# Performance work log

Measured on AMD Instinct MI355X. Metric: run time of the kernel, lower is better.

## Reference

```python
import jax, jax.numpy as jnp
import numpy as np
from jax.scipy.special import logsumexp

NG, NF, NR, NW = 5, 5, 5, 4
STEP = 1 + NG + NF + NR            # 16 signatures per writer
M_OTH = NG + NF + NR               # comparisons per writer
MARGIN, RANDOM_MARGIN = 1.0, 1.5
ALPHA, BETA, P_W, R_W = 0.1, 1.0, 0.01, 0.01
GAMMA = 5.0                        # SoftDTW(gamma=5, bandwidth=int(0.1)=0 -> full DTW)
KNUM, KMUL = 5, 2.0
MAXLEN, FEAT = 512, 64
BIG = 1e10                         # finite stand-in for +inf (exp(-BIG/GAMMA) == 0 in f32)


def _pairwise_sqdist(X, Y):
    # X,Y: (B, L, F) -> (B, L, L) squared euclidean cost (SoftDTW distance func)
    xy = jnp.einsum('bif,bjf->bij', X, Y)
    d = (X * X).sum(-1)[:, :, None] + (Y * Y).sum(-1)[:, None, :] - 2.0 * xy
    return jnp.maximum(d, 0.0)


def _soft_dtw(D, la, lb):
    # Batched soft-DTW via anti-diagonal scan. Padded DP is causal, so
    # R[la, lb] only depends on D[:la, :lb]; padding never contaminates it.
    B, L, _ = D.shape
    ii = jnp.arange(1, L + 1)
    r2 = jnp.full((B, L + 1), BIG, D.dtype).at[:, 0].set(0.0)  # diag d=0: R[0,0]=0
    r1 = jnp.full((B, L + 1), BIG, D.dtype)                    # diag d=1: borders

    def step(carry, d):
        rp2, rp1 = carry
        j = d - ii
        valid = (j >= 1) & (j <= L)
        jc = jnp.clip(j, 1, L)
        Dd = D[:, ii - 1, jc - 1]                               # (B, L)
        # softmin(R[i-1,j], R[i,j-1], R[i-1,j-1]) = -g*logsumexp(-r/g)
        stack = jnp.stack([-rp1[:, :-1], -rp1[:, 1:], -rp2[:, :-1]]) / GAMMA
        smin = -GAMMA * logsumexp(stack, axis=0)
        vals = jnp.where(valid[None, :], Dd + smin, BIG)
        r_new = jnp.concatenate([jnp.full((B, 1), BIG, D.dtype), vals], axis=1)
        return (rp1, r_new), r_new

    _, R = jax.lax.scan(step, (r2, r1), jnp.arange(2, 2 * L + 1))
    # R: (2L-1, B, L+1); diag d stored at d-2, R[la, lb] sits at index la
    return R[la + lb - 2, jnp.arange(B), la]


def _mmd(src, tgt):
    # DAN-style multi-kernel gaussian MMD; signatures flattened to vectors
    b = src.shape[0]
    total = jnp.concatenate([src, tgt], axis=0)
    n = total.shape[0]
    sq = (total * total).sum(-1)
    l2 = jnp.maximum(sq[:, None] + sq[None, :] - 2.0 * (total @ total.T), 0.0)
    bw = jax.lax.stop_gradient(l2.sum()) / (n * n - n)
    bw = bw / KMUL ** (KNUM // 2)
    bws = bw * KMUL ** jnp.arange(KNUM, dtype=total.dtype)
    k = jnp.exp(-l2[None] / bws[:, None, None]).sum(0)
    return jnp.mean(k[:b, :b] + k[b:, b:] - k[:b, b:] - k[b:, :b])


def _forward(data, lens):
    w = jnp.arange(NW)
    anchor_idx = jnp.repeat(w * STEP, M_OTH)
    other_idx = (w[:, None] * STEP + 1 + jnp.arange(M_OTH)[None, :]).reshape(-1)
    D = _pairwise_sqdist(data[anchor_idx], data[other_idx])
    la, lb = lens[anchor_idx], lens[other_idx]
    r = _soft_dtw(D, la, lb)
    dists = (r / (la + lb).astype(data.dtype)).reshape(NW, M_OTH)  # avg pooling
    dist_g = dists[:, :NG]
    dist_n = dists[:, NG:]
    lk_s = jax.nn.relu(dist_g[:, :, None] + MARGIN - dist_n[:, None, :NF])
    lk_r = jax.nn.relu(dist_g[:, :, None] + RANDOM_MARGIN - dist_n[:, None, NF:])
    ca = dist_g.mean(1)
    cb = dist_n[:, :NW].mean(1)            # quirk of original: first nw negatives
    intra = (dist_g - ca[:, None]).sum(1)  # identically 0, kept for fidelity
    inter = jax.nn.relu(BETA - jnp.abs(ca - cb))
    nz_s = (lk_s > 0).sum((1, 2))
    nz_r = (lk_r > 0).sum((1, 2))
    lv = (lk_s.sum((1, 2)) + lk_r.sum((1, 2))) / (nz_s + nz_r + 1)
    # BCE over softmin pairs (dist_g[0], dist_r[j]) vs targets (1, 0):
    # softmin gives sm0 = sigmoid(dr - dg0); BCE = -(log sm0 + log(1-sm1))/2 = -log sm0
    logits = dist_n[:, NF:] - dist_g[:, 0:1]
    bce = -jnp.mean(jax.nn.log_sigmoid(logits), axis=1)
    total_loss = jnp.mean(bce + lv + intra * P_W + inter * R_W)
    # pairwise MMD over writers (i in 0..nw-1, j in 1..nw-1, i != j), nr random excluded
    pairs = np.array([(i, j) for i in range(NW) for j in range(1, NW) if i != j])
    seg = data.reshape(NW, STEP, MAXLEN, FEAT)[:, :STEP - NR]
    seg = seg.reshape(NW, STEP - NR, MAXLEN * FEAT)
    mmd_vals = jax.vmap(_mmd)(seg[pairs[:, 0]], seg[pairs[:, 1]])
    siz = NW * (NW + 1) // 2
    mmds = jnp.zeros((siz,), data.dtype).at[:pairs.shape[0]].set(mmd_vals)
    mmd1 = jnp.max(mmds) * ALPHA
    return total_loss + mmd1, nz_r.sum()


def setup_inputs():
    key = jax.random.key(0)
    k1, k2, k3 = jax.random.split(key, 3)
    data = jax.random.normal(k1, (NW * STEP, MAXLEN, FEAT), dtype=jnp.float32)
    lens = jax.random.randint(k2, (NW * STEP,), MAXLEN // 2, MAXLEN + 1, dtype=jnp.int32)
    target = jax.random.randint(k3, (NW * STEP,), 0, NW, dtype=jnp.int32)
    return {"data": data, "lens": lens, "target": target, "n_classes": 100}


def reference(data, lens, target, n_classes):
    # target / n_classes are unused in the original forward (sms is dead code)
    return _forward(data, lens)
```

## Files before the change

kernel.cpp:

```cpp
#include <hip/hip_runtime.h>
#include <math.h>

#define NG 5
#define NF 5
#define NR 5
#define NW 4
#define STEP 16
#define M_OTH 15
#define NB 60
#define L 512
#define FEAT 64
#define GAMMA 5.0f
#define SEGN 11
#define NSEG 44
#define SEGD 32768

#define C1   0.28853900817779268f
#define GLN2 3.4657359027997265f
#define BIGS 2.8853900e9f
#define BNDW 792
#define GRAM_BLK0 60

__global__ __launch_bounds__(256, 2) void sqdist_kernel(const float* __restrict__ data,
                                                        float* __restrict__ DS) {
    int b = blockIdx.z;
    int w = b / M_OTH, m = b % M_OTH;
    const float* X = data + (size_t)(w * STEP) * L * FEAT;
    const float* Y = data + (size_t)(w * STEP + 1 + m) * L * FEAT;
    int ti = blockIdx.y * 128;
    int tj = blockIdx.x * 128;

    __shared__ float Xs[128][68];
    __shared__ float Ys[128][68];
    __shared__ float nx[128], ny[128];

    int t = threadIdx.y * 16 + threadIdx.x;
    #pragma unroll
    for (int k = 0; k < 8; ++k) {
        int idx = t + k * 256;
        int r = idx >> 4, c = (idx & 15) * 4;
        *(float4*)&Xs[r][c] = *(const float4*)(X + (size_t)(ti + r) * FEAT + c);
        *(float4*)&Ys[r][c] = *(const float4*)(Y + (size_t)(tj + r) * FEAT + c);
    }
    __syncthreads();
    {
        int r = t & 127;
        const float* row = (t < 128) ? Xs[r] : Ys[r];
        float s = 0.f;
        #pragma unroll
        for (int f = 0; f < 64; f += 4) {
            float4 v = *(const float4*)&row[f];
            s += v.x * v.x + v.y * v.y + v.z * v.z + v.w * v.w;
        }
        if (t < 128) nx[r] = s; else ny[r] = s;
    }
    __syncthreads();

    int tx = threadIdx.x, ty = threadIdx.y;
    float acc[8][8] = {};
    for (int f = 0; f < 64; f += 4) {
        float4 xv[8], yv[8];
        #pragma unroll
        for (int a = 0; a < 8; ++a) xv[a] = *(const float4*)&Xs[16 * a + tx][f];
        #pragma unroll
        for (int c = 0; c < 8; ++c) yv[c] = *(const float4*)&Ys[16 * c + ty][f];
        #pragma unroll
        for (int a = 0; a < 8; ++a)
            #pragma unroll
            for (int c = 0; c < 8; ++c)
                acc[a][c] += xv[a].x * yv[c].x + xv[a].y * yv[c].y +
                             xv[a].z * yv[c].z + xv[a].w * yv[c].w;
    }
    #pragma unroll
    for (int a = 0; a < 8; ++a) {
        int ii = ti + 16 * a + tx;
        float xn = nx[16 * a + tx];
        #pragma unroll
        for (int c = 0; c < 8; ++c) {
            int jj = tj + 16 * c + ty;
            float d = xn + ny[16 * c + ty] - 2.0f * acc[a][c];
            size_t idx = ((size_t)b * 512 + ((jj + (ii >> 1)) & 511)) * 512 + ii;
            DS[idx] = fmaxf(d, 0.0f) * C1;
        }
    }
}

__device__ __forceinline__ float dpp_shift_up1(float x) {
    int xi = __float_as_int(x);
    int sh  = __builtin_amdgcn_update_dpp(xi, xi, 0x111, 0xF, 0xF, false);
    int b15 = __builtin_amdgcn_update_dpp(xi, xi, 0x142, 0xF, 0xF, false);
    int lane = (int)(threadIdx.x & 63);
    int r = ((lane & 15) == 0) ? b15 : sh;
    return __int_as_float(r);
}

__device__ void gram_body(const float* __restrict__ data, float* __restrict__ Gm, int f) {
    int bx = 0, rem = f;
    for (int q = 0; q < 11; ++q) { int c = 11 - q; if (rem < c) { bx = q; break; } rem -= c; }
    int by = bx + rem;
    int t = threadIdx.x;
    int lane = t & 63, wv = t >> 6;
    const float* pa[4];
    const float* pb[4];
    #pragma unroll
    for (int i = 0; i < 4; ++i) {
        int sa = bx * 4 + i;
        int sb = by * 4 + i;
        pa[i] = data + (size_t)((sa / SEGN) * STEP + (sa % SEGN)) * SEGD;
        pb[i] = data + (size_t)((sb / SEGN) * STEP + (sb % SEGN)) * SEGD;
    }
    float acc[16] = {};
    for (int d = t * 4; d < SEGD; d += 1024) {
        float4 ra[4], rb[4];
        #pragma unroll
        for (int i = 0; i < 4; ++i) ra[i] = *(const float4*)(pa[i] + d);
        #pragma unroll
        for (int i = 0; i < 4; ++i) rb[i] = *(const float4*)(pb[i] + d);
        #pragma unroll
        for (int i = 0; i < 4; ++i)
            #pragma unroll
            for (int jj = 0; jj < 4; ++jj)
                acc[i * 4 + jj] += ra[i].x * rb[jj].x + ra[i].y * rb[jj].y +
                                   ra[i].z * rb[jj].z + ra[i].w * rb[jj].w;
    }
    #pragma unroll
    for (int i = 0; i < 16; ++i)
        #pragma unroll
        for (int s = 32; s > 0; s >>= 1)
            acc[i] += __shfl_xor(acc[i], s);
    __shared__ float part[4][16];
    if (lane == 0)
        #pragma unroll
        for (int i = 0; i < 16; ++i) part[wv][i] = acc[i];
    __syncthreads();
    if (t < 16) {
        float s = part[0][t] + part[1][t] + part[2][t] + part[3][t];
        int a = bx * 4 + (t >> 2), c = by * 4 + (t & 3);
        Gm[a * NSEG + c] = s;
        Gm[c * NSEG + a] = s;
    }
}

__global__ __launch_bounds__(256) void dtw_gram_kernel(const float* __restrict__ DS,
                                                       const int* __restrict__ lens,
                                                       const float* __restrict__ data,
                                                       float* __restrict__ res,
                                                       float* __restrict__ Gm) {
    int blk = blockIdx.x;
    if (blk >= GRAM_BLK0) { gram_body(data, Gm, blk - GRAM_BLK0); return; }

    int b = blk;
    int w_ = b / M_OTH, m = b % M_OTH;
    int la = lens[w_ * STEP];
    int lb = lens[w_ * STEP + 1 + m];
    int tid = threadIdx.x;
    int W = tid >> 6, l = tid & 63, G = tid;
    const float* Db = DS + (size_t)b * 512 * 512;

    __shared__ float bnd[3][BNDW];
    for (int k = tid; k < 3 * BNDW; k += 256)
        ((float*)bnd)[k] = __int_as_float(0x7FC00000);
    __syncthreads();

    int gstar = (la - 1) >> 1;
    int rstar = (la - 1) & 1;
    int tcap = lb + gstar - 1;
    if (64 * W > gstar) return;
    int gmax = min(64 * W + 63, gstar);
    int t0 = 64 * W;
    int tend = lb + gmax - 1;
    int needmax = lb + 64 * W - 1;
    bool pub = (W < 3);

    float nv0 = BIGS, nv1 = BIGS;
    float A0 = BIGS;
    float C0 = (G == 0) ? 0.0f : BIGS;
    float out = 0.0f;

    float2 ring[8];
    #pragma unroll
    for (int k = 0; k < 8; ++k)
        ring[k] = *(const float2*)&Db[(size_t)((t0 + k) & 511) * 512 + 2 * G];
    float ch[8];
    #pragma unroll
    for (int k = 0; k < 8; ++k) ch[k] = __int_as_float(0x7FC00000);

    int j = 1 - l;
    const float* bsrc = (W > 0) ? bnd[W - 1] : bnd[0];

    for (int t = t0; t <= tend; t += 8) {
        if (W > 0 && t <= needmax) {
            int lastIdx = min(t + 7, needmax);
            bool full = (t + 7 <= needmax);
            bool ok = full && !__builtin_isnan(ch[3]) && !__builtin_isnan(ch[7]);
            if (!ok) {
                float v = __hip_atomic_load(&bsrc[lastIdx], __ATOMIC_RELAXED,
                                            __HIP_MEMORY_SCOPE_WORKGROUP);
                while (__builtin_isnan(v)) {
                    __builtin_amdgcn_s_sleep(2);
                    v = __hip_atomic_load(&bsrc[lastIdx], __ATOMIC_RELAXED,
                                          __HIP_MEMORY_SCOPE_WORKGROUP);
                }
                __builtin_amdgcn_fence(__ATOMIC_ACQUIRE, "workgroup");
                #pragma unroll
                for (int k = 0; k < 8; ++k)
                    ch[k] = __hip_atomic_load(&bsrc[t + k], __ATOMIC_RELAXED,
                                              __HIP_MEMORY_SCOPE_WORKGROUP);
            }
        }
        #pragma unroll
        for (int k = 0; k < 8; ++k) {
            int tt = t + k;
            float l0 = BIGS;
            if (W > 0) l0 = (tt <= needmax) ? ch[k] : BIGS;
            A0 = (l == 0) ? l0 : A0;
            float D0 = ring[k].x, D1 = ring[k].y;
            ring[k] = *(const float2*)&Db[(size_t)((tt + 8) & 511) * 512 + 2 * G];
            float m2a = fminf(nv0, C0), mxa = fmaxf(nv0, C0);
            float E2a = 1.0f + __builtin_amdgcn_exp2f(m2a - mxa);
            float m2b = fminf(nv1, nv0), mxb = fmaxf(nv1, nv0);
            float E2b = 1.0f + __builtin_amdgcn_exp2f(m2b - mxb);
            float mn0 = fminf(A0, m2a);
            float s0 = __builtin_amdgcn_exp2f(mn0 - A0) +
                       E2a * __builtin_amdgcn_exp2f(mn0 - m2a);
            float t0v = D0 + (mn0 - __builtin_amdgcn_logf(s0));
            float mn1 = fminf(t0v, m2b);
            float s1 = __builtin_amdgcn_exp2f(mn1 - t0v) +
                       E2b * __builtin_amdgcn_exp2f(mn1 - m2b);
            float t1v = D1 + (mn1 - __builtin_amdgcn_logf(s1));
            bool valid = (unsigned)(j - 1) < (unsigned)L;
            nv0 = valid ? t0v : nv0;
            nv1 = valid ? t1v : nv1;
            if (tt == tcap) { if (G == gstar) out = rstar ? nv1 : nv0; }
            float up = dpp_shift_up1(nv1);
            if (pub && l == 63)
                __hip_atomic_store(&bnd[W][tt + 1], nv1, __ATOMIC_RELAXED,
                                   __HIP_MEMORY_SCOPE_WORKGROUP);
            C0 = A0;
            A0 = up;
            j += 1;
        }
        if (W > 0) {
            float4 ca = *(const float4*)&bsrc[t + 8];
            float4 cb = *(const float4*)&bsrc[t + 12];
            ch[0] = ca.x; ch[1] = ca.y; ch[2] = ca.z; ch[3] = ca.w;
            ch[4] = cb.x; ch[5] = cb.y; ch[6] = cb.z; ch[7] = cb.w;
        }
    }
    if (G == gstar) res[b] = out * GLN2 / (float)(la + lb);
}

__global__ __launch_bounds__(512) void finalize_kernel(const float* __restrict__ res,
                                                       const float* __restrict__ G,
                                                       float* __restrict__ out) {
    __shared__ float wpart[9][8];
    __shared__ float bws[9];
    __shared__ float mmds[9];
    __shared__ float wloss[NW];
    __shared__ int   wnzr[NW];
    int t = threadIdx.x, lane = t & 63, wv = t >> 6;

    if (t < NW) {
        int w = t;
        float dg[NG], dn[NF + NR];
        for (int g = 0; g < NG; ++g) dg[g] = res[w * M_OTH + g];
        for (int q = 0; q < NF + NR; ++q) dn[q] = res[w * M_OTH + NG + q];
        float sum_s = 0.f, sum_r = 0.f;
        int nzs = 0, nzr = 0;
        for (int g = 0; g < NG; ++g) {
            for (int f = 0; f < NF; ++f) {
                float v = dg[g] + 1.0f - dn[f];
                if (v > 0.f) { sum_s += v; nzs++; }
            }
            for (int r = 0; r < NR; ++r) {
                float v = dg[g] + 1.5f - dn[NF + r];
                if (v > 0.f) { sum_r += v; nzr++; }
            }
        }
        float ca = (dg[0] + dg[1] + dg[2] + dg[3] + dg[4]) / 5.0f;
        float cb = (dn[0] + dn[1] + dn[2] + dn[3]) * 0.25f;
        float intra = 0.f;
        for (int g = 0; g < NG; ++g) intra += dg[g] - ca;
        float inter = fmaxf(0.f, 1.0f - fabsf(ca - cb));
        float lv = (sum_s + sum_r) / (float)(nzs + nzr + 1);
        float bce = 0.f;
        for (int r = 0; r < NR; ++r) {
            float x = dn[NF + r] - dg[0];
            float ls = (x >= 0.f) ? -log1pf(expf(-x)) : (x - log1pf(expf(x)));
            bce += ls;
        }
        bce = -bce / 5.0f;
        wloss[w] = bce + lv + intra * 0.01f + inter * 0.01f;
        wnzr[w] = nzr;
    }

    const int pi[9] = {0, 0, 0, 1, 1, 2, 2, 3, 3};
    const int pj[9] = {1, 2, 3, 2, 3, 1, 3, 1, 2};
    int pp = t / 22, qq = t % 22;
    bool act = t < 484;
    float l2v[9];
    #pragma unroll
    for (int p = 0; p < 9; ++p) {
        float v = 0.f;
        if (act) {
            int wi = pi[p], wj = pj[p];
            int gp = (pp < 11) ? wi * SEGN + pp : wj * SEGN + (pp - 11);
            int gq = (qq < 11) ? wi * SEGN + qq : wj * SEGN + (qq - 11);
            v = fmaxf(G[gp * NSEG + gp] + G[gq * NSEG + gq] - 2.f * G[gp * NSEG + gq], 0.f);
        }
        l2v[p] = v;
    }
    #pragma unroll
    for (int p = 0; p < 9; ++p) {
        float r = l2v[p];
        #pragma unroll
        for (int s = 32; s > 0; s >>= 1) r += __shfl_xor(r, s);
        if (lane == 0) wpart[p][wv] = r;
    }
    __syncthreads();
    if (t < 9) {
        float s = 0.f;
        #pragma unroll
        for (int k = 0; k < 8; ++k) s += wpart[t][k];
        bws[t] = s * (1.0f / 462.0f) * 0.25f;
    }
    __syncthreads();
    float sgn = ((pp < 11) == (qq < 11)) ? 1.f : -1.f;
    #pragma unroll
    for (int p = 0; p < 9; ++p) {
        float kv = 0.f;
        if (act) {
            float x = -l2v[p] / bws[p];
            kv = sgn * (__expf(x) + __expf(x * 0.5f) + __expf(x * 0.25f) +
                        __expf(x * 0.125f) + __expf(x * 0.0625f));
        }
        #pragma unroll
        for (int s = 32; s > 0; s >>= 1) kv += __shfl_xor(kv, s);
        if (lane == 0) wpart[p][wv] = kv;
    }
    __syncthreads();
    if (t < 9) {
        float s = 0.f;
        #pragma unroll
        for (int k = 0; k < 8; ++k) s += wpart[t][k];
        mmds[t] = s / 121.0f;
    }
    __syncthreads();
    if (t == 0) {
        float loss = 0.25f * (wloss[0] + wloss[1] + wloss[2] + wloss[3]);
        float mx = 0.f;
        for (int p = 0; p < 9; ++p) mx = fmaxf(mx, mmds[p]);
        out[0] = loss + 0.1f * mx;
        out[1] = (float)(wnzr[0] + wnzr[1] + wnzr[2] + wnzr[3]);
    }
}

extern "C" void kernel_launch(void* const* d_in, const int* in_sizes, int n_in,
                              void* d_out, int out_size, void* d_ws, size_t ws_size,
                              hipStream_t stream) {
    const float* data = (const float*)d_in[0];
    const int* lens = (const int*)d_in[1];

    float* DS  = (float*)d_ws;
    float* res = DS + (size_t)NB * 512 * 512;
    float* G   = res + 64;
    float* out = (float*)d_out;

    dim3 g1(4, 4, NB), b1(16, 16);
    sqdist_kernel<<<g1, b1, 0, stream>>>(data, DS);
    dtw_gram_kernel<<<GRAM_BLK0 + 66, 256, 0, stream>>>(DS, lens, data, res, G);
    finalize_kernel<<<1, 512, 0, stream>>>(res, G, out);
}
```

Before: 164.0 us.

## Pack two DTW problems per block, skip out-of-length sqdist tiles, trim softmin exps

```diff
diff --git a/kernel.cpp b/kernel.cpp
--- a/kernel.cpp
+++ b/kernel.cpp
@@ -18,17 +18,22 @@
 #define C1   0.28853900817779268f
 #define GLN2 3.4657359027997265f
 #define BIGS 2.8853900e9f
-#define BNDW 792
-#define GRAM_BLK0 60
+#define BNDW 800
+#define DTW_BLKS 30
 
 __global__ __launch_bounds__(256, 2) void sqdist_kernel(const float* __restrict__ data,
+                                                        const int* __restrict__ lens,
                                                         float* __restrict__ DS) {
     int b = blockIdx.z;
     int w = b / M_OTH, m = b % M_OTH;
+    int la = lens[w * STEP];
+    int lb = lens[w * STEP + 1 + m];
+    int ti = blockIdx.y * 128;
+    int tj = blockIdx.x * 128;
+    if (ti >= la || tj >= lb) return;
+
     const float* X = data + (size_t)(w * STEP) * L * FEAT;
     const float* Y = data + (size_t)(w * STEP + 1 + m) * L * FEAT;
-    int ti = blockIdx.y * 128;
-    int tj = blockIdx.x * 128;
 
     __shared__ float Xs[128][68];
     __shared__ float Ys[128][68];
@@ -110,7 +115,7 @@
         pb[i] = data + (size_t)((sb / SEGN) * STEP + (sb % SEGN)) * SEGD;
     }
     float acc[16] = {};
-    for (int d = t * 4; d < SEGD; d += 1024) {
+    for (int d = t * 4; d < SEGD; d += 2048) {
         float4 ra[4], rb[4];
         #pragma unroll
         for (int i = 0; i < 4; ++i) ra[i] = *(const float4*)(pa[i] + d);
@@ -128,39 +133,43 @@
         #pragma unroll
         for (int s = 32; s > 0; s >>= 1)
             acc[i] += __shfl_xor(acc[i], s);
-    __shared__ float part[4][16];
+    __shared__ float part[8][16];
     if (lane == 0)
         #pragma unroll
         for (int i = 0; i < 16; ++i) part[wv][i] = acc[i];
     __syncthreads();
     if (t < 16) {
-        float s = part[0][t] + part[1][t] + part[2][t] + part[3][t];
+        float s = 0.f;
+        #pragma unroll
+        for (int k = 0; k < 8; ++k) s += part[k][t];
         int a = bx * 4 + (t >> 2), c = by * 4 + (t & 3);
         Gm[a * NSEG + c] = s;
         Gm[c * NSEG + a] = s;
     }
 }
 
-__global__ __launch_bounds__(256) void dtw_gram_kernel(const float* __restrict__ DS,
+__global__ __launch_bounds__(512) void dtw_gram_kernel(const float* __restrict__ DS,
                                                        const int* __restrict__ lens,
                                                        const float* __restrict__ data,
                                                        float* __restrict__ res,
                                                        float* __restrict__ Gm) {
     int blk = blockIdx.x;
-    if (blk >= GRAM_BLK0) { gram_body(data, Gm, blk - GRAM_BLK0); return; }
-
-    int b = blk;
+    if (blk >= DTW_BLKS) { gram_body(data, Gm, blk - DTW_BLKS); return; }
+
+    __shared__ float bnd[2][3][BNDW];
+    int tid = threadIdx.x;
+    for (int k = tid; k < 2 * 3 * BNDW; k += 512)
+        ((float*)bnd)[k] = __int_as_float(0x7FC00000);
+    __syncthreads();
+
+    int P = tid >> 8;
+    int q = tid & 255;
+    int W = q >> 6, l = tid & 63, G = q;
+    int b = blk * 2 + P;
     int w_ = b / M_OTH, m = b % M_OTH;
     int la = lens[w_ * STEP];
     int lb = lens[w_ * STEP + 1 + m];
-    int tid = threadIdx.x;
-    int W = tid >> 6, l = tid & 63, G = tid;
     const float* Db = DS + (size_t)b * 512 * 512;
-
-    __shared__ float bnd[3][BNDW];
-    for (int k = tid; k < 3 * BNDW; k += 256)
-        ((float*)bnd)[k] = __int_as_float(0x7FC00000);
-    __syncthreads();
 
     int gstar = (la - 1) >> 1;
     int rstar = (la - 1) & 1;
@@ -186,19 +195,19 @@
     for (int k = 0; k < 8; ++k) ch[k] = __int_as_float(0x7FC00000);
 
     int j = 1 - l;
-    const float* bsrc = (W > 0) ? bnd[W - 1] : bnd[0];
+    const float* bsrc = (W > 0) ? bnd[P][W - 1] : bnd[P][0];
 
     for (int t = t0; t <= tend; t += 8) {
         if (W > 0 && t <= needmax) {
-            int lastIdx = min(t + 7, needmax);
-            bool full = (t + 7 <= needmax);
-            bool ok = full && !__builtin_isnan(ch[3]) && !__builtin_isnan(ch[7]);
+            bool ok = (t + 7 <= needmax) && !__builtin_isnan(ch[3]) &&
+                      !__builtin_isnan(ch[7]);
             if (!ok) {
-                float v = __hip_atomic_load(&bsrc[lastIdx], __ATOMIC_RELAXED,
+                int pollIdx = min(t + 15, needmax);
+                float v = __hip_atomic_load(&bsrc[pollIdx], __ATOMIC_RELAXED,
                                             __HIP_MEMORY_SCOPE_WORKGROUP);
                 while (__builtin_isnan(v)) {
                     __builtin_amdgcn_s_sleep(2);
-                    v = __hip_atomic_load(&bsrc[lastIdx], __ATOMIC_RELAXED,
+                    v = __hip_atomic_load(&bsrc[pollIdx], __ATOMIC_RELAXED,
                                           __HIP_MEMORY_SCOPE_WORKGROUP);
                 }
                 __builtin_amdgcn_fence(__ATOMIC_ACQUIRE, "workgroup");
@@ -218,15 +227,15 @@
             ring[k] = *(const float2*)&Db[(size_t)((tt + 8) & 511) * 512 + 2 * G];
             float m2a = fminf(nv0, C0), mxa = fmaxf(nv0, C0);
             float E2a = 1.0f + __builtin_amdgcn_exp2f(m2a - mxa);
+            float mn0 = fminf(A0, m2a), mx0 = fmaxf(A0, m2a);
+            float e0 = __builtin_amdgcn_exp2f(mn0 - mx0);
+            float s0 = (A0 <= m2a) ? fmaf(E2a, e0, 1.0f) : (e0 + E2a);
+            float t0v = D0 + (mn0 - __builtin_amdgcn_logf(s0));
             float m2b = fminf(nv1, nv0), mxb = fmaxf(nv1, nv0);
             float E2b = 1.0f + __builtin_amdgcn_exp2f(m2b - mxb);
-            float mn0 = fminf(A0, m2a);
-            float s0 = __builtin_amdgcn_exp2f(mn0 - A0) +
-                       E2a * __builtin_amdgcn_exp2f(mn0 - m2a);
-            float t0v = D0 + (mn0 - __builtin_amdgcn_logf(s0));
-            float mn1 = fminf(t0v, m2b);
-            float s1 = __builtin_amdgcn_exp2f(mn1 - t0v) +
-                       E2b * __builtin_amdgcn_exp2f(mn1 - m2b);
+            float mn1 = fminf(t0v, m2b), mx1 = fmaxf(t0v, m2b);
+            float e1 = __builtin_amdgcn_exp2f(mn1 - mx1);
+            float s1 = (t0v <= m2b) ? fmaf(E2b, e1, 1.0f) : (e1 + E2b);
             float t1v = D1 + (mn1 - __builtin_amdgcn_logf(s1));
             bool valid = (unsigned)(j - 1) < (unsigned)L;
             nv0 = valid ? t0v : nv0;
@@ -234,7 +243,7 @@
             if (tt == tcap) { if (G == gstar) out = rstar ? nv1 : nv0; }
             float up = dpp_shift_up1(nv1);
             if (pub && l == 63)
-                __hip_atomic_store(&bnd[W][tt + 1], nv1, __ATOMIC_RELAXED,
+                __hip_atomic_store(&bnd[P][W][tt + 1], nv1, __ATOMIC_RELAXED,
                                    __HIP_MEMORY_SCOPE_WORKGROUP);
             C0 = A0;
             A0 = up;
@@ -264,7 +273,7 @@
         int w = t;
         float dg[NG], dn[NF + NR];
         for (int g = 0; g < NG; ++g) dg[g] = res[w * M_OTH + g];
-        for (int q = 0; q < NF + NR; ++q) dn[q] = res[w * M_OTH + NG + q];
+        for (int qq2 = 0; qq2 < NF + NR; ++qq2) dn[qq2] = res[w * M_OTH + NG + qq2];
         float sum_s = 0.f, sum_r = 0.f;
         int nzs = 0, nzr = 0;
         for (int g = 0; g < NG; ++g) {
@@ -367,7 +376,7 @@
     float* out = (float*)d_out;
 
     dim3 g1(4, 4, NB), b1(16, 16);
-    sqdist_kernel<<<g1, b1, 0, stream>>>(data, DS);
-    dtw_gram_kernel<<<GRAM_BLK0 + 66, 256, 0, stream>>>(DS, lens, data, res, G);
+    sqdist_kernel<<<g1, b1, 0, stream>>>(data, lens, DS);
+    dtw_gram_kernel<<<DTW_BLKS + 66, 512, 0, stream>>>(DS, lens, data, res, G);
     finalize_kernel<<<1, 512, 0, stream>>>(res, G, out);
 }
```

Measured after the change: 215.3 us. +31.3%, slower.

## Carry DTW state as (log-offset, scale) pairs and skip sqdist tiles past lengths

Applied to the files above, without the earlier changes.

```diff
diff --git a/kernel.cpp b/kernel.cpp
--- a/kernel.cpp
+++ b/kernel.cpp
@@ -18,17 +18,25 @@
 #define C1   0.28853900817779268f
 #define GLN2 3.4657359027997265f
 #define BIGS 2.8853900e9f
-#define BNDW 792
+#define BNDW 800
 #define GRAM_BLK0 60
+#define SENT 0x7FC000007FC00000ULL
+
+typedef struct __align__(16) { unsigned long long x, y; } ull2_t;
 
 __global__ __launch_bounds__(256, 2) void sqdist_kernel(const float* __restrict__ data,
+                                                        const int* __restrict__ lens,
                                                         float* __restrict__ DS) {
     int b = blockIdx.z;
     int w = b / M_OTH, m = b % M_OTH;
+    int la = lens[w * STEP];
+    int lb = lens[w * STEP + 1 + m];
+    int ti = blockIdx.y * 128;
+    int tj = blockIdx.x * 128;
+    if (ti >= la || tj >= lb) return;
+
     const float* X = data + (size_t)(w * STEP) * L * FEAT;
     const float* Y = data + (size_t)(w * STEP + 1 + m) * L * FEAT;
-    int ti = blockIdx.y * 128;
-    int tj = blockIdx.x * 128;
 
     __shared__ float Xs[128][68];
     __shared__ float Ys[128][68];
@@ -157,9 +165,9 @@
     int W = tid >> 6, l = tid & 63, G = tid;
     const float* Db = DS + (size_t)b * 512 * 512;
 
-    __shared__ float bnd[3][BNDW];
+    __shared__ unsigned long long bnd[3][BNDW];
     for (int k = tid; k < 3 * BNDW; k += 256)
-        ((float*)bnd)[k] = __int_as_float(0x7FC00000);
+        ((unsigned long long*)bnd)[k] = SENT;
     __syncthreads();
 
     int gstar = (la - 1) >> 1;
@@ -172,31 +180,34 @@
     int needmax = lb + 64 * W - 1;
     bool pub = (W < 3);
 
-    float nv0 = BIGS, nv1 = BIGS;
-    float A0 = BIGS;
-    float C0 = (G == 0) ? 0.0f : BIGS;
-    float out = 0.0f;
+    float p0 = BIGS, s0 = 1.f;
+    float p1 = BIGS, s1 = 1.f;
+    float pA = BIGS, sA = 1.f;
+    float pC = (G == 0) ? 0.f : BIGS;
+    float sC = 1.f;
+    float outp = 0.f, outs = 1.f;
 
     float2 ring[8];
     #pragma unroll
     for (int k = 0; k < 8; ++k)
         ring[k] = *(const float2*)&Db[(size_t)((t0 + k) & 511) * 512 + 2 * G];
-    float ch[8];
-    #pragma unroll
-    for (int k = 0; k < 8; ++k) ch[k] = __int_as_float(0x7FC00000);
+    unsigned long long ch[8];
+    #pragma unroll
+    for (int k = 0; k < 8; ++k) ch[k] = SENT;
 
     int j = 1 - l;
-    const float* bsrc = (W > 0) ? bnd[W - 1] : bnd[0];
+    const unsigned long long* bsrc = (W > 0) ? bnd[W - 1] : bnd[0];
 
     for (int t = t0; t <= tend; t += 8) {
         if (W > 0 && t <= needmax) {
-            int lastIdx = min(t + 7, needmax);
-            bool full = (t + 7 <= needmax);
-            bool ok = full && !__builtin_isnan(ch[3]) && !__builtin_isnan(ch[7]);
+            bool ok = (t + 7 <= needmax) &&
+                      !__builtin_isnan(__int_as_float((int)(unsigned)ch[3])) &&
+                      !__builtin_isnan(__int_as_float((int)(unsigned)ch[7]));
             if (!ok) {
-                float v = __hip_atomic_load(&bsrc[lastIdx], __ATOMIC_RELAXED,
-                                            __HIP_MEMORY_SCOPE_WORKGROUP);
-                while (__builtin_isnan(v)) {
+                int lastIdx = min(t + 7, needmax);
+                unsigned long long v = __hip_atomic_load(&bsrc[lastIdx], __ATOMIC_RELAXED,
+                                                         __HIP_MEMORY_SCOPE_WORKGROUP);
+                while (__builtin_isnan(__int_as_float((int)(unsigned)v))) {
                     __builtin_amdgcn_s_sleep(2);
                     v = __hip_atomic_load(&bsrc[lastIdx], __ATOMIC_RELAXED,
                                           __HIP_MEMORY_SCOPE_WORKGROUP);
@@ -211,43 +222,60 @@
         #pragma unroll
         for (int k = 0; k < 8; ++k) {
             int tt = t + k;
-            float l0 = BIGS;
-            if (W > 0) l0 = (tt <= needmax) ? ch[k] : BIGS;
-            A0 = (l == 0) ? l0 : A0;
+            float l0p = BIGS, l0s = 1.0f;
+            if (W > 0 && tt <= needmax) {
+                l0p = __int_as_float((int)(unsigned)ch[k]);
+                l0s = __int_as_float((int)(unsigned)(ch[k] >> 32));
+            }
+            pA = (l == 0) ? l0p : pA;
+            sA = (l == 0) ? l0s : sA;
             float D0 = ring[k].x, D1 = ring[k].y;
             ring[k] = *(const float2*)&Db[(size_t)((tt + 8) & 511) * 512 + 2 * G];
-            float m2a = fminf(nv0, C0), mxa = fmaxf(nv0, C0);
-            float E2a = 1.0f + __builtin_amdgcn_exp2f(m2a - mxa);
-            float m2b = fminf(nv1, nv0), mxb = fmaxf(nv1, nv0);
-            float E2b = 1.0f + __builtin_amdgcn_exp2f(m2b - mxb);
-            float mn0 = fminf(A0, m2a);
-            float s0 = __builtin_amdgcn_exp2f(mn0 - A0) +
-                       E2a * __builtin_amdgcn_exp2f(mn0 - m2a);
-            float t0v = D0 + (mn0 - __builtin_amdgcn_logf(s0));
-            float mn1 = fminf(t0v, m2b);
-            float s1 = __builtin_amdgcn_exp2f(mn1 - t0v) +
-                       E2b * __builtin_amdgcn_exp2f(mn1 - m2b);
-            float t1v = D1 + (mn1 - __builtin_amdgcn_logf(s1));
+            float mbc = fminf(p0, pC), xbc = fmaxf(p0, pC);
+            float ebc = __builtin_amdgcn_exp2f(mbc - xbc);
+            float E2  = (p0 <= pC) ? fmaf(ebc, sC, s0) : fmaf(ebc, s0, sC);
+            float ref0 = fminf(pA, mbc), mx0 = fmaxf(pA, mbc);
+            float e0 = __builtin_amdgcn_exp2f(ref0 - mx0);
+            float s0n = (pA <= mbc) ? fmaf(e0, E2, sA) : fmaf(e0, sA, E2);
+            float p0n = D0 + ref0;
+            float mbc1 = fminf(p1, p0), xbc1 = fmaxf(p1, p0);
+            float ebc1 = __builtin_amdgcn_exp2f(mbc1 - xbc1);
+            float E2b = (p1 <= p0) ? fmaf(ebc1, s0, s1) : fmaf(ebc1, s1, s0);
+            float ref1 = fminf(p0n, mbc1), mx1 = fmaxf(p0n, mbc1);
+            float e1 = __builtin_amdgcn_exp2f(ref1 - mx1);
+            float s1n = (p0n <= mbc1) ? fmaf(e1, E2b, s0n) : fmaf(e1, s0n, E2b);
+            float p1n = D1 + ref1;
             bool valid = (unsigned)(j - 1) < (unsigned)L;
-            nv0 = valid ? t0v : nv0;
-            nv1 = valid ? t1v : nv1;
-            if (tt == tcap) { if (G == gstar) out = rstar ? nv1 : nv0; }
-            float up = dpp_shift_up1(nv1);
-            if (pub && l == 63)
-                __hip_atomic_store(&bnd[W][tt + 1], nv1, __ATOMIC_RELAXED,
+            p0 = valid ? p0n : p0;  s0 = valid ? s0n : s0;
+            p1 = valid ? p1n : p1;  s1 = valid ? s1n : s1;
+            if (tt == tcap) {
+                if (G == gstar) { outp = rstar ? p1 : p0; outs = rstar ? s1 : s0; }
+            }
+            float upP = dpp_shift_up1(p1);
+            float upS = dpp_shift_up1(s1);
+            if (pub && l == 63) {
+                union { float2 f; unsigned long long u; } pk;
+                pk.f = make_float2(p1, s1);
+                __hip_atomic_store(&bnd[W][tt + 1], pk.u, __ATOMIC_RELAXED,
                                    __HIP_MEMORY_SCOPE_WORKGROUP);
-            C0 = A0;
-            A0 = up;
+            }
+            pC = pA; sC = sA;
+            pA = upP; sA = upS;
             j += 1;
         }
+        if ((t & 8) != 0) {
+            p0 -= __builtin_amdgcn_logf(s0); s0 = 1.0f;
+            p1 -= __builtin_amdgcn_logf(s1); s1 = 1.0f;
+        }
         if (W > 0) {
-            float4 ca = *(const float4*)&bsrc[t + 8];
-            float4 cb = *(const float4*)&bsrc[t + 12];
-            ch[0] = ca.x; ch[1] = ca.y; ch[2] = ca.z; ch[3] = ca.w;
-            ch[4] = cb.x; ch[5] = cb.y; ch[6] = cb.z; ch[7] = cb.w;
-        }
-    }
-    if (G == gstar) res[b] = out * GLN2 / (float)(la + lb);
+            const ull2_t* sp = (const ull2_t*)&bsrc[t + 8];
+            ull2_t c0 = sp[0], c1 = sp[1], c2 = sp[2], c3 = sp[3];
+            ch[0] = c0.x; ch[1] = c0.y; ch[2] = c1.x; ch[3] = c1.y;
+            ch[4] = c2.x; ch[5] = c2.y; ch[6] = c3.x; ch[7] = c3.y;
+        }
+    }
+    if (G == gstar)
+        res[b] = (outp - __builtin_amdgcn_logf(outs)) * GLN2 / (float)(la + lb);
 }
 
 __global__ __launch_bounds__(512) void finalize_kernel(const float* __restrict__ res,
@@ -264,7 +292,7 @@
         int w = t;
         float dg[NG], dn[NF + NR];
         for (int g = 0; g < NG; ++g) dg[g] = res[w * M_OTH + g];
-        for (int q = 0; q < NF + NR; ++q) dn[q] = res[w * M_OTH + NG + q];
+        for (int q2 = 0; q2 < NF + NR; ++q2) dn[q2] = res[w * M_OTH + NG + q2];
         float sum_s = 0.f, sum_r = 0.f;
         int nzs = 0, nzr = 0;
         for (int g = 0; g < NG; ++g) {
@@ -367,7 +395,7 @@
     float* out = (float*)d_out;
 
     dim3 g1(4, 4, NB), b1(16, 16);
-    sqdist_kernel<<<g1, b1, 0, stream>>>(data, DS);
+    sqdist_kernel<<<g1, b1, 0, stream>>>(data, lens, DS);
     dtw_gram_kernel<<<GRAM_BLK0 + 66, 256, 0, stream>>>(DS, lens, data, res, G);
     finalize_kernel<<<1, 512, 0, stream>>>(res, G, out);
 }
```

Result: slower. 185.0 us (+12.8%).
